# Kernel tuning notes

Measured on AMD Instinct MI355X. Metric: run time of the kernel, lower is better.

The kernel has to match this reference:

```python
import jax, jax.numpy as jnp
import numpy as np

NEG_SLOPE = 0.2  # GATv2Conv default negative_slope
EPS = 1e-5       # BatchNorm1d default eps


def _bn(x, g, b):
    # training-mode batch norm (biased variance, matching torch normalization)
    m = x.mean(0)
    v = x.var(0)
    return (x - m) / jnp.sqrt(v + EPS) * g + b


def setup_inputs() -> dict:
    key = jax.random.key(0)
    N, E, AIN, EIN, HID, H, OUT = 50000, 400000, 64, 16, 64, 8, 1
    ks = jax.random.split(key, 16)
    def nrm(k, shape, s=0.05):
        return jax.random.normal(k, shape, jnp.float32) * s
    return dict(
        x=nrm(ks[0], (N, AIN), 1.0),
        edge_index=jax.random.randint(ks[1], (2, E), 0, N),
        edge_attr=nrm(ks[2], (E, EIN), 1.0),
        W_ap=nrm(ks[3], (AIN, HID)), b_ap=jnp.zeros((HID,), jnp.float32),
        W_ep=nrm(ks[4], (EIN, HID)), b_ep=jnp.zeros((HID,), jnp.float32),
        W_msg=nrm(ks[5], (HID, HID)), b_msg=jnp.zeros((HID,), jnp.float32),
        g_msg=jnp.ones((HID,), jnp.float32), be_msg=jnp.zeros((HID,), jnp.float32),
        W_l=nrm(ks[6], (2 * HID, H * HID)), W_r=nrm(ks[7], (2 * HID, H * HID)),
        att=nrm(ks[8], (H, HID)), b_gat=jnp.zeros((H * HID,), jnp.float32),
        g_bn=jnp.ones((H * HID,), jnp.float32), be_bn=jnp.zeros((H * HID,), jnp.float32),
        W_p1=nrm(ks[9], (H * HID, HID)), b_p1=jnp.zeros((HID,), jnp.float32),
        g_p=jnp.ones((HID,), jnp.float32), be_p=jnp.zeros((HID,), jnp.float32),
        W_p2=nrm(ks[10], (HID, OUT)), b_p2=jnp.zeros((OUT,), jnp.float32),
    )


def reference(x, edge_index, edge_attr,
              W_ap, b_ap, W_ep, b_ep, W_msg, b_msg, g_msg, be_msg,
              W_l, W_r, att, b_gat, g_bn, be_bn,
              W_p1, b_p1, g_p, be_p, W_p2, b_p2):
    N = x.shape[0]
    H, C = att.shape
    row, col = edge_index[0], edge_index[1]

    atom = x @ W_ap + b_ap                      # [N, HID]
    ef = edge_attr @ W_ep + b_ep                # [E, HID]

    # scatter_mean of edge features onto destination nodes
    s = jax.ops.segment_sum(ef, col, num_segments=N)
    cnt = jax.ops.segment_sum(jnp.ones((ef.shape[0],), ef.dtype), col, num_segments=N)
    agg = s / jnp.clip(cnt, 1.0)[:, None]       # [N, HID]

    msg = jax.nn.relu(_bn((atom + agg) @ W_msg + b_msg, g_msg, be_msg))
    comb = jnp.concatenate([msg, agg], axis=1)  # [N, 2*HID]

    # GATv2Conv with default add_self_loops=True, concat=True
    src = jnp.concatenate([row, jnp.arange(N, dtype=row.dtype)])
    dst = jnp.concatenate([col, jnp.arange(N, dtype=col.dtype)])
    xl = (comb @ W_l).reshape(N, H, C)          # source transform
    xr = (comb @ W_r).reshape(N, H, C)          # target transform
    e = jax.nn.leaky_relu(xl[src] + xr[dst], NEG_SLOPE)   # [E+N, H, C]
    score = jnp.einsum('ehc,hc->eh', e, att)               # [E+N, H]
    smax = jax.ops.segment_max(score, dst, num_segments=N)
    ex = jnp.exp(score - smax[dst])
    denom = jax.ops.segment_sum(ex, dst, num_segments=N)
    alpha = ex / denom[dst]                                 # per-dst softmax
    out = jax.ops.segment_sum(alpha[:, :, None] * xl[src], dst, num_segments=N)
    out = out.reshape(N, H * C) + b_gat                     # [N, H*C]

    out = jax.nn.relu(_bn(out, g_bn, be_bn))
    h = jax.nn.relu(_bn(out @ W_p1 + b_p1, g_p, be_p))
    return (h @ W_p2 + b_p2).squeeze(-1)                    # [N]
```

## Files before the change

### kernel.cpp

```cpp
#include <hip/hip_runtime.h>
#include <hip/hip_bf16.h>


#define CDIV(a, b) (((a) + (b) - 1) / (b))

using f32x4 = __attribute__((ext_vector_type(4))) float;
using s16x8 = __attribute__((ext_vector_type(8))) short;
using u32x4 = __attribute__((ext_vector_type(4))) unsigned;

__device__ inline unsigned short f2bf(float f) {
    union { float f; unsigned u; } v; v.f = f;
    unsigned r = v.u + 0x7fff + ((v.u >> 16) & 1);
    return (unsigned short)(r >> 16);
}
__device__ inline float bf_lo(unsigned w) {
    union { unsigned u; float f; } v; v.u = w << 16; return v.f;
}
__device__ inline float bf_hi(unsigned w) {
    union { unsigned u; float f; } v; v.u = w & 0xffff0000u; return v.f;
}
__device__ inline void unp8(u32x4 u, float* v) {
    v[0] = bf_lo(u.x); v[1] = bf_hi(u.x); v[2] = bf_lo(u.y); v[3] = bf_hi(u.y);
    v[4] = bf_lo(u.z); v[5] = bf_hi(u.z); v[6] = bf_lo(u.w); v[7] = bf_hi(u.w);
}

__global__ void k_scatter16(const float* __restrict__ EA, const int* __restrict__ ei,
                            float* __restrict__ agg16, int* __restrict__ cntI, int E) {
    int t = blockIdx.x * blockDim.x + threadIdx.x;
    int e = t >> 4, ch = t & 15;
    if (e >= E) return;
    int dst = ei[E + e];
    float v = __builtin_nontemporal_load(EA + (size_t)e * 16 + ch);
    atomicAdd(&agg16[(size_t)dst * 16 + ch], v);
    if (ch == 0) atomicAdd(&cntI[dst], 1);
}

__global__ void k_prep(const float* __restrict__ Wl, const float* __restrict__ Wr,
                       const float* __restrict__ Wp1, const float* __restrict__ Wap,
                       const float* __restrict__ Wmsg, const float* __restrict__ bap,
                       const float* __restrict__ bmsg, unsigned short* __restrict__ Wt,
                       unsigned short* __restrict__ Wp1t, unsigned short* __restrict__ Wzt,
                       float* __restrict__ bc) {
    int b = blockIdx.x, t = threadIdx.x;
    if (b < 512) {
        int idx = b * 256 + t;
        int c = idx >> 7, k = idx & 127;
        float v = (c < 512) ? Wl[(size_t)k * 512 + c] : Wr[(size_t)k * 512 + (c - 512)];
        Wt[idx] = f2bf(v);
    } else if (b < 640) {
        int idx = (b - 512) * 256 + t;
        int c = idx >> 9, k = idx & 511;
        Wp1t[idx] = f2bf(Wp1[(size_t)k * 64 + c]);
    } else {
        for (int e = t; e < 4096; e += 256) {
            int i = e >> 6, c = e & 63;
            float s = 0.f;
            for (int j = 0; j < 64; ++j) s += Wap[i * 64 + j] * Wmsg[j * 64 + c];
            Wzt[c * 128 + i] = f2bf(s);
        }
        for (int e = t; e < 4096; e += 256) {
            int k = e >> 6, c = e & 63;
            Wzt[c * 128 + 64 + k] = f2bf(Wmsg[k * 64 + c]);
        }
        if (t < 64) {
            float s = bmsg[t];
            for (int j = 0; j < 64; ++j) s += bap[j] * Wmsg[j * 64 + t];
            bc[t] = s;
        }
    }
}

__global__ void k_combin(const float* __restrict__ x, const float* __restrict__ agg16,
                         const int* __restrict__ cntI, const float* __restrict__ Wep,
                         const float* __restrict__ bep, unsigned* __restrict__ combin32,
                         int N) {
    int wid = (blockIdx.x * blockDim.x + threadIdx.x) >> 6;
    int lane = threadIdx.x & 63;
    if (wid >= N) return;
    int c = cntI[wid];
    float mval = (lane < 16 && c > 0) ? agg16[(size_t)wid * 16 + lane] / (float)c : 0.f;
    float aggv = bep[lane];
#pragma unroll
    for (int j = 0; j < 16; ++j) {
        float mj = __shfl(mval, j, 64);
        aggv = fmaf(mj, Wep[j * 64 + lane], aggv);
    }
    if (c == 0) aggv = 0.f;
    float xv = __builtin_nontemporal_load(x + (size_t)wid * 64 + lane);
    int i0 = (lane & 31) * 2;
    float ax = __shfl(xv, i0, 64);
    float bx = __shfl(xv, i0 + 1, 64);
    float aa = __shfl(aggv, i0, 64);
    float ba = __shfl(aggv, i0 + 1, 64);
    float a = (lane < 32) ? ax : aa;
    float b = (lane < 32) ? bx : ba;
    combin32[(size_t)wid * 64 + lane] = (unsigned)f2bf(a) | ((unsigned)f2bf(b) << 16);
}

__global__ __launch_bounds__(256) void k_z(
    const unsigned short* __restrict__ combin, const unsigned short* __restrict__ Wzt,
    const float* __restrict__ bc, float* __restrict__ z, float* __restrict__ sums, int N) {
    __shared__ unsigned short a_lds[64 * 128];
    __shared__ unsigned short b_lds[64 * 128];
    __shared__ float redS[64], redQ[64];
    int t = threadIdx.x;
    int row0 = blockIdx.x * 64;
    for (int i = t; i < 1024; i += 256) {
        int row = i >> 4, seg = i & 15;
        int dsts = (row * 256 + ((seg * 16) ^ ((row & 7) << 4))) >> 1;
        int gr = row0 + row;
        s16x8 v = (s16x8)0;
        if (gr < N) v = *(const s16x8*)(combin + (size_t)gr * 128 + seg * 8);
        *(s16x8*)(a_lds + dsts) = v;
        *(s16x8*)(b_lds + dsts) = *(const s16x8*)(Wzt + (size_t)row * 128 + seg * 8);
    }
    if (t < 64) { redS[t] = 0.f; redQ[t] = 0.f; }
    __syncthreads();
    int w = t >> 6, l = t & 63, hi = l >> 4, lo = l & 15;
    int ar = w * 16 + lo;
    s16x8 a[4];
#pragma unroll
    for (int kk = 0; kk < 4; ++kk) {
        int byte = (kk * 64 + hi * 16) ^ ((ar & 7) << 4);
        a[kk] = *(const s16x8*)(a_lds + ((ar * 256 + byte) >> 1));
    }
#pragma unroll
    for (int cf = 0; cf < 4; ++cf) {
        int br = cf * 16 + lo;
        f32x4 acc = (f32x4){0.f, 0.f, 0.f, 0.f};
#pragma unroll
        for (int kk = 0; kk < 4; ++kk) {
            int byte = (kk * 64 + hi * 16) ^ ((br & 7) << 4);
            s16x8 b = *(const s16x8*)(b_lds + ((br * 256 + byte) >> 1));
            acc = __builtin_amdgcn_mfma_f32_16x16x32_bf16(a[kk], b, acc, 0, 0, 0);
        }
        int colg = cf * 16 + lo;
        float bcv = bc[colg];
        float sv = 0.f, qv = 0.f;
#pragma unroll
        for (int r = 0; r < 4; ++r) {
            int rowg = row0 + w * 16 + hi * 4 + r;
            if (rowg < N) {
                float v = acc[r] + bcv;
                z[(size_t)rowg * 64 + colg] = v;
                sv += v; qv += v * v;
            }
        }
        atomicAdd(&redS[colg], sv);
        atomicAdd(&redQ[colg], qv);
    }
    __syncthreads();
    if (t < 64) {
        atomicAdd(&sums[t], redS[t]);
        atomicAdd(&sums[64 + t], redQ[t]);
    }
}

__global__ __launch_bounds__(256) void k_statsg(const u32x4* __restrict__ X,
                                                float* __restrict__ sums, int N) {
    __shared__ float redS[512], redQ[512];
    int t = threadIdx.x;
    for (int i = t; i < 512; i += 256) { redS[i] = 0.f; redQ[i] = 0.f; }
    __syncthreads();
    int qu = t & 63;
    int slice = (blockIdx.x << 2) | (t >> 6);
    int nsl = gridDim.x << 2;
    float s[8], q[8];
#pragma unroll
    for (int j = 0; j < 8; ++j) { s[j] = 0.f; q[j] = 0.f; }
    for (int n = slice; n < N; n += nsl) {
        u32x4 u = X[(size_t)n * 64 + qu];
        unsigned uu[4] = {u.x, u.y, u.z, u.w};
#pragma unroll
        for (int k2 = 0; k2 < 4; ++k2) {
            float a = bf_lo(uu[k2]), b = bf_hi(uu[k2]);
            s[2 * k2] += a; q[2 * k2] += a * a;
            s[2 * k2 + 1] += b; q[2 * k2 + 1] += b * b;
        }
    }
#pragma unroll
    for (int j = 0; j < 8; ++j) {
        atomicAdd(&redS[qu * 8 + j], s[j]);
        atomicAdd(&redQ[qu * 8 + j], q[j]);
    }
    __syncthreads();
    for (int i = t; i < 512; i += 256) {
        atomicAdd(&sums[i], redS[i]);
        atomicAdd(&sums[512 + i], redQ[i]);
    }
}

__global__ void k_comb2(const float* __restrict__ z, const float* __restrict__ sums,
                        const float* __restrict__ g, const float* __restrict__ be,
                        unsigned* __restrict__ combin32, int N) {
    int idx = blockIdx.x * blockDim.x + threadIdx.x;
    if (idx >= N * 16) return;
    int n = idx >> 4, kq = idx & 15;
    float invN = 1.0f / (float)N;
    float4 zv = *(const float4*)(z + (size_t)n * 64 + kq * 4);
    float zz[4] = {zv.x, zv.y, zv.z, zv.w};
    unsigned h[2];
#pragma unroll
    for (int p = 0; p < 2; ++p) {
        unsigned short w[2];
#pragma unroll
        for (int j = 0; j < 2; ++j) {
            int k = kq * 4 + p * 2 + j;
            float mean = sums[k] * invN;
            float var = sums[64 + k] * invN - mean * mean;
            float s = g[k] * rsqrtf(var + 1e-5f);
            float v = fmaxf(fmaf(zz[p * 2 + j], s, be[k] - mean * s), 0.f);
            w[j] = f2bf(v);
        }
        h[p] = (unsigned)w[0] | ((unsigned)w[1] << 16);
    }
    *(uint2*)(combin32 + (size_t)n * 64 + kq * 2) = make_uint2(h[0], h[1]);
}

__global__ void k_bsum(const int* __restrict__ cntI, int* __restrict__ bsum, int N) {
    int b = blockIdx.x, t = threadIdx.x;
    int base = b * 1024 + t * 4;
    int s = 0;
#pragma unroll
    for (int j = 0; j < 4; ++j) { int i = base + j; if (i < N) s += cntI[i]; }
    for (int off = 32; off; off >>= 1) s += __shfl_xor(s, off, 64);
    __shared__ int wsum[4];
    if ((t & 63) == 0) wsum[t >> 6] = s;
    __syncthreads();
    if (t == 0) bsum[b] = wsum[0] + wsum[1] + wsum[2] + wsum[3];
}
__global__ void k_boff(const int* __restrict__ bsum, int* __restrict__ boff, int nb) {
    int t = threadIdx.x;
    if (t < nb) { int s = 0; for (int j = 0; j < t; ++j) s += bsum[j]; boff[t] = s; }
}
__global__ void k_scan2(const int* __restrict__ cntI, const int* __restrict__ boff,
                        int* __restrict__ rowptr, int N) {
    int b = blockIdx.x, t = threadIdx.x;
    int base = b * 1024 + t * 4;
    int v[4]; int s = 0;
#pragma unroll
    for (int j = 0; j < 4; ++j) { int i = base + j; v[j] = (i < N) ? cntI[i] : 0; s += v[j]; }
    __shared__ int ls[256];
    ls[t] = s; __syncthreads();
    for (int off = 1; off < 256; off <<= 1) {
        int tv = (t >= (int)off) ? ls[t - off] : 0;
        __syncthreads(); ls[t] += tv; __syncthreads();
    }
    int run = ls[t] - s + boff[b];
#pragma unroll
    for (int j = 0; j < 4; ++j) { run += v[j]; int i = base + j; if (i < N) rowptr[i + 1] = run; }
    if (b == 0 && t == 0) rowptr[0] = 0;
}

__global__ void k_fill(const int* __restrict__ ei, const int* __restrict__ rowptr,
                       int* __restrict__ cursor, int* __restrict__ esrc, int E) {
    int e = blockIdx.x * blockDim.x + threadIdx.x;
    if (e >= E) return;
    int dst = ei[E + e];
    int pos = rowptr[dst] + atomicAdd(&cursor[dst], 1);
    esrc[pos] = ei[e];
}

__global__ __launch_bounds__(256) void k_xlxr2(
    const unsigned short* __restrict__ combin, const unsigned short* __restrict__ Wt,
    unsigned short* __restrict__ xlr, int N) {
    __shared__ unsigned short a_lds[64 * 128];
    __shared__ unsigned short b_lds[256 * 128];
    int t = threadIdx.x;
    int row0 = blockIdx.x * 64;
    int c0 = blockIdx.y * 256;
    for (int i = t; i < 1024; i += 256) {
        int row = i >> 4, seg = i & 15;
        int dsts = (row * 256 + ((seg * 16) ^ ((row & 7) << 4))) >> 1;
        int gr = row0 + row;
        s16x8 v = (s16x8)0;
        if (gr < N) v = *(const s16x8*)(combin + (size_t)gr * 128 + seg * 8);
        *(s16x8*)(a_lds + dsts) = v;
    }
    for (int i = t; i < 4096; i += 256) {
        int row = i >> 4, seg = i & 15;
        int dsts = (row * 256 + ((seg * 16) ^ ((row & 7) << 4))) >> 1;
        *(s16x8*)(b_lds + dsts) = *(const s16x8*)(Wt + (size_t)(c0 + row) * 128 + seg * 8);
    }
    __syncthreads();
    int w = t >> 6, l = t & 63, hi = l >> 4, lo = l & 15;
    int ar = w * 16 + lo;
    s16x8 a[4];
#pragma unroll
    for (int kk = 0; kk < 4; ++kk) {
        int byte = (kk * 64 + hi * 16) ^ ((ar & 7) << 4);
        a[kk] = *(const s16x8*)(a_lds + ((ar * 256 + byte) >> 1));
    }
#pragma unroll
    for (int cf = 0; cf < 16; ++cf) {
        int br = cf * 16 + lo;
        f32x4 acc = (f32x4){0.f, 0.f, 0.f, 0.f};
#pragma unroll
        for (int kk = 0; kk < 4; ++kk) {
            int byte = (kk * 64 + hi * 16) ^ ((br & 7) << 4);
            s16x8 b = *(const s16x8*)(b_lds + ((br * 256 + byte) >> 1));
            acc = __builtin_amdgcn_mfma_f32_16x16x32_bf16(a[kk], b, acc, 0, 0, 0);
        }
        int colg = c0 + cf * 16 + lo;
#pragma unroll
        for (int r = 0; r < 4; ++r) {
            int rowg = row0 + w * 16 + hi * 4 + r;
            if (rowg < N) xlr[(size_t)rowg * 1024 + colg] = f2bf(acc[r]);
        }
    }
}

__global__ __launch_bounds__(256) void k_gat(
    const unsigned short* __restrict__ xlr, unsigned* __restrict__ gout32,
    const int* __restrict__ rowptr, const int* __restrict__ esrc,
    const float* __restrict__ att, const float* __restrict__ bg, int N) {
    int wid = (blockIdx.x * blockDim.x + threadIdx.x) >> 6;
    int lane = threadIdx.x & 63;
    if (wid >= N) return;
    int n = wid;
    float xrv[8], av[8], acc[8];
    {
        u32x4 u = __builtin_nontemporal_load(
            (const u32x4*)(xlr + (size_t)n * 1024 + 512 + lane * 8));
        unp8(u, xrv);
    }
#pragma unroll
    for (int j = 0; j < 8; ++j) { av[j] = att[lane * 8 + j]; acc[j] = 0.f; }
    float s = 0.f;
    int e0 = rowptr[n], e1 = rowptr[n + 1];
    int m = e1 - e0 + 1;
    int i = 0;
    for (; i + 2 <= m; i += 2) {
        int ia = e0 + i, ib = e0 + i + 1;
        int s0 = (ia < e1) ? esrc[ia] : n;
        int s1 = (ib < e1) ? esrc[ib] : n;
        u32x4 u0 = *(const u32x4*)(xlr + (size_t)s0 * 1024 + lane * 8);
        u32x4 u1 = *(const u32x4*)(xlr + (size_t)s1 * 1024 + lane * 8);
        float xlv0[8], xlv1[8];
        unp8(u0, xlv0); unp8(u1, xlv1);
        float ps0 = 0.f, ps1 = 0.f;
#pragma unroll
        for (int j = 0; j < 8; ++j) {
            float t0 = xlv0[j] + xrv[j];
            float t1 = xlv1[j] + xrv[j];
            t0 = fmaf(0.4f, fabsf(t0), 0.6f * t0);
            t1 = fmaf(0.4f, fabsf(t1), 0.6f * t1);
            ps0 = fmaf(t0, av[j], ps0);
            ps1 = fmaf(t1, av[j], ps1);
        }
        ps0 += __shfl_xor(ps0, 1, 64); ps1 += __shfl_xor(ps1, 1, 64);
        ps0 += __shfl_xor(ps0, 2, 64); ps1 += __shfl_xor(ps1, 2, 64);
        ps0 += __shfl_xor(ps0, 4, 64); ps1 += __shfl_xor(ps1, 4, 64);
        float w0 = __expf(ps0), w1 = __expf(ps1);
        s += w0 + w1;
#pragma unroll
        for (int j = 0; j < 8; ++j) {
            acc[j] = fmaf(w0, xlv0[j], acc[j]);
            acc[j] = fmaf(w1, xlv1[j], acc[j]);
        }
    }
    if (i < m) {
        int ia = e0 + i;
        int s0 = (ia < e1) ? esrc[ia] : n;
        u32x4 u0 = *(const u32x4*)(xlr + (size_t)s0 * 1024 + lane * 8);
        float xlv0[8];
        unp8(u0, xlv0);
        float ps0 = 0.f;
#pragma unroll
        for (int j = 0; j < 8; ++j) {
            float t0 = xlv0[j] + xrv[j];
            t0 = fmaf(0.4f, fabsf(t0), 0.6f * t0);
            ps0 = fmaf(t0, av[j], ps0);
        }
        ps0 += __shfl_xor(ps0, 1, 64);
        ps0 += __shfl_xor(ps0, 2, 64);
        ps0 += __shfl_xor(ps0, 4, 64);
        float w0 = __expf(ps0);
        s += w0;
#pragma unroll
        for (int j = 0; j < 8; ++j) acc[j] = fmaf(w0, xlv0[j], acc[j]);
    }
    float invs = 1.0f / s;
    u32x4 o;
    {
        float lo0 = acc[0] * invs + bg[lane * 8 + 0];
        float hi0 = acc[1] * invs + bg[lane * 8 + 1];
        float lo1 = acc[2] * invs + bg[lane * 8 + 2];
        float hi1 = acc[3] * invs + bg[lane * 8 + 3];
        float lo2 = acc[4] * invs + bg[lane * 8 + 4];
        float hi2 = acc[5] * invs + bg[lane * 8 + 5];
        float lo3 = acc[6] * invs + bg[lane * 8 + 6];
        float hi3 = acc[7] * invs + bg[lane * 8 + 7];
        o.x = (unsigned)f2bf(lo0) | ((unsigned)f2bf(hi0) << 16);
        o.y = (unsigned)f2bf(lo1) | ((unsigned)f2bf(hi1) << 16);
        o.z = (unsigned)f2bf(lo2) | ((unsigned)f2bf(hi2) << 16);
        o.w = (unsigned)f2bf(lo3) | ((unsigned)f2bf(hi3) << 16);
    }
    __builtin_nontemporal_store(o, (u32x4*)(gout32 + (size_t)n * 256 + lane * 4));
}

__global__ __launch_bounds__(256) void k_postm(
    const unsigned* __restrict__ gout32, const unsigned short* __restrict__ Wp1t,
    const float* __restrict__ gsums, const float* __restrict__ g,
    const float* __restrict__ be, const float* __restrict__ bp1,
    float* __restrict__ h1, float* __restrict__ sums, int N) {
    __shared__ unsigned short a_lds[64 * 128];
    __shared__ unsigned short b_lds[64 * 128];
    __shared__ float sc_l[512], sh_l[512];
    __shared__ float redS[64], redQ[64];
    int t = threadIdx.x;
    float invN = 1.0f / (float)N;
    for (int i = t; i < 512; i += 256) {
        float mean = gsums[i] * invN;
        float var = gsums[512 + i] * invN - mean * mean;
        float s = g[i] * rsqrtf(var + 1e-5f);
        sc_l[i] = s;
        sh_l[i] = be[i] - mean * s;
    }
    if (t < 64) { redS[t] = 0.f; redQ[t] = 0.f; }
    int row0 = blockIdx.x * 64;
    int w = t >> 6, l = t & 63, hi = l >> 4, lo = l & 15;
    int ar = w * 16 + lo;
    f32x4 acc[4];
#pragma unroll
    for (int cf = 0; cf < 4; ++cf) acc[cf] = (f32x4){0.f, 0.f, 0.f, 0.f};
    for (int kc = 0; kc < 4; ++kc) {
        __syncthreads();
        for (int i = t; i < 1024; i += 256) {
            int row = i >> 4, seg = i & 15;
            int dsts = (row * 256 + ((seg * 16) ^ ((row & 7) << 4))) >> 1;
            int gr = row0 + row;
            int k0 = kc * 128 + seg * 8;
            s16x8 v = (s16x8)0;
            if (gr < N) {
                u32x4 u = *(const u32x4*)(gout32 + (size_t)gr * 256 + (k0 >> 1));
                float f[8];
                unp8(u, f);
#pragma unroll
                for (int j = 0; j < 8; ++j) {
                    float y = fmaxf(fmaf(f[j], sc_l[k0 + j], sh_l[k0 + j]), 0.f);
                    v[j] = (short)f2bf(y);
                }
            }
            *(s16x8*)(a_lds + dsts) = v;
            *(s16x8*)(b_lds + dsts) = *(const s16x8*)(Wp1t + (size_t)row * 512 + k0);
        }
        __syncthreads();
        s16x8 a[4];
#pragma unroll
        for (int kk = 0; kk < 4; ++kk) {
            int byte = (kk * 64 + hi * 16) ^ ((ar & 7) << 4);
            a[kk] = *(const s16x8*)(a_lds + ((ar * 256 + byte) >> 1));
        }
#pragma unroll
        for (int cf = 0; cf < 4; ++cf) {
            int br = cf * 16 + lo;
#pragma unroll
            for (int kk = 0; kk < 4; ++kk) {
                int byte = (kk * 64 + hi * 16) ^ ((br & 7) << 4);
                s16x8 b = *(const s16x8*)(b_lds + ((br * 256 + byte) >> 1));
                acc[cf] = __builtin_amdgcn_mfma_f32_16x16x32_bf16(a[kk], b, acc[cf], 0, 0, 0);
            }
        }
    }
#pragma unroll
    for (int cf = 0; cf < 4; ++cf) {
        int colg = cf * 16 + lo;
        float bv = bp1[colg];
        float sv = 0.f, qv = 0.f;
#pragma unroll
        for (int r = 0; r < 4; ++r) {
            int rowg = row0 + w * 16 + hi * 4 + r;
            if (rowg < N) {
                float v = acc[cf][r] + bv;
                h1[(size_t)rowg * 64 + colg] = v;
                sv += v; qv += v * v;
            }
        }
        atomicAdd(&redS[colg], sv);
        atomicAdd(&redQ[colg], qv);
    }
    __syncthreads();
    if (t < 64) {
        atomicAdd(&sums[t], redS[t]);
        atomicAdd(&sums[64 + t], redQ[t]);
    }
}

__global__ void k_final(const float* __restrict__ h1, const float* __restrict__ stats,
                        const float* __restrict__ g, const float* __restrict__ be,
                        const float* __restrict__ Wp2, const float* __restrict__ bp2,
                        float* __restrict__ out, int N) {
    int wid = (blockIdx.x * blockDim.x + threadIdx.x) >> 6;
    int lane = threadIdx.x & 63;
    if (wid >= N) return;
    float invN = 1.0f / (float)N;
    float mean = stats[lane] * invN;
    float var = stats[64 + lane] * invN - mean * mean;
    float inv = rsqrtf(var + 1e-5f);
    float v = h1[(size_t)wid * 64 + lane];
    v = fmaxf((v - mean) * (inv * g[lane]) + be[lane], 0.f);
    float p = v * Wp2[lane];
#pragma unroll
    for (int off = 32; off; off >>= 1) p += __shfl_xor(p, off, 64);
    if (lane == 0) out[wid] = p + bp2[0];
}

extern "C" void kernel_launch(void* const* d_in, const int* in_sizes, int n_in,
                              void* d_out, int out_size, void* d_ws, size_t ws_size,
                              hipStream_t stream) {
    const float* x      = (const float*)d_in[0];
    const int*   ei     = (const int*)d_in[1];
    const float* ea     = (const float*)d_in[2];
    const float* W_ap   = (const float*)d_in[3];
    const float* b_ap   = (const float*)d_in[4];
    const float* W_ep   = (const float*)d_in[5];
    const float* b_ep   = (const float*)d_in[6];
    const float* W_msg  = (const float*)d_in[7];
    const float* b_msg  = (const float*)d_in[8];
    const float* g_msg  = (const float*)d_in[9];
    const float* be_msg = (const float*)d_in[10];
    const float* W_l    = (const float*)d_in[11];
    const float* W_r    = (const float*)d_in[12];
    const float* att    = (const float*)d_in[13];
    const float* b_gat  = (const float*)d_in[14];
    const float* g_bn   = (const float*)d_in[15];
    const float* be_bn  = (const float*)d_in[16];
    const float* W_p1   = (const float*)d_in[17];
    const float* b_p1   = (const float*)d_in[18];
    const float* g_p    = (const float*)d_in[19];
    const float* be_p   = (const float*)d_in[20];
    const float* W_p2   = (const float*)d_in[21];
    const float* b_p2   = (const float*)d_in[22];

    int N = in_sizes[0] / 64;
    int E = in_sizes[1] / 2;
    int nb = CDIV(N, 1024);

    float* ws = (float*)d_ws;
    size_t off = 0;
    float* agg16  = ws + off; off += (size_t)N * 16;
    int*   cntI   = (int*)(ws + off); off += N;
    int*   cursor = (int*)(ws + off); off += N;
    float* st_msg = ws + off; off += 128;
    float* st_gat = ws + off; off += 1024;
    float* st_p   = ws + off; off += 128;
    size_t zero_floats = off;
    unsigned short* combin = (unsigned short*)(ws + off); off += (size_t)N * 64;
    float* zb     = ws + off; off += (size_t)N * 64;
    unsigned short* Wzt = (unsigned short*)(ws + off); off += 4096;
    float* bc     = ws + off; off += 64;
    int*   rowptr = (int*)(ws + off); off += (size_t)(N + 1); off = (off + 3) & ~(size_t)3;
    int*   esrc   = (int*)(ws + off); off += E;
    int*   bsum   = (int*)(ws + off); off += 64;
    int*   boff   = (int*)(ws + off); off += 64;
    unsigned short* Wt  = (unsigned short*)(ws + off); off += 65536;
    unsigned short* Wp1t = (unsigned short*)(ws + off); off += 16384;
    unsigned short* xlr = (unsigned short*)(ws + off); off += (size_t)N * 512;
    unsigned* gout32 = (unsigned*)(ws + off); off += (size_t)N * 256;
    float* h1 = zb;

    hipMemsetAsync(d_ws, 0, zero_floats * sizeof(float), stream);

    k_prep<<<641, 256, 0, stream>>>(W_l, W_r, W_p1, W_ap, W_msg, b_ap, b_msg,
                                    Wt, Wp1t, Wzt, bc);
    k_scatter16<<<CDIV(E * 16, 256), 256, 0, stream>>>(ea, ei, agg16, cntI, E);
    k_combin<<<CDIV(N * 64, 256), 256, 0, stream>>>(x, agg16, cntI, W_ep, b_ep,
                                                    (unsigned*)combin, N);
    k_z<<<CDIV(N, 64), 256, 0, stream>>>(combin, Wzt, bc, zb, st_msg, N);
    k_comb2<<<CDIV(N * 16, 256), 256, 0, stream>>>(zb, st_msg, g_msg, be_msg,
                                                   (unsigned*)combin, N);
    k_bsum<<<nb, 256, 0, stream>>>(cntI, bsum, N);
    k_boff<<<1, 64, 0, stream>>>(bsum, boff, nb);
    k_scan2<<<nb, 256, 0, stream>>>(cntI, boff, rowptr, N);
    k_fill<<<CDIV(E, 256), 256, 0, stream>>>(ei, rowptr, cursor, esrc, E);
    dim3 gx(CDIV(N, 64), 4);
    k_xlxr2<<<gx, 256, 0, stream>>>(combin, Wt, xlr, N);
    k_gat<<<CDIV(N * 64, 256), 256, 0, stream>>>(xlr, gout32, rowptr, esrc, att, b_gat, N);
    k_statsg<<<256, 256, 0, stream>>>((const u32x4*)gout32, st_gat, N);
    k_postm<<<CDIV(N, 64), 256, 0, stream>>>(gout32, Wp1t, st_gat, g_bn, be_bn,
                                             b_p1, h1, st_p, N);
    k_final<<<CDIV(N * 64, 256), 256, 0, stream>>>(h1, st_p, g_p, be_p, W_p2, b_p2,
                                                   (float*)d_out, N);
}
```

Before: 408.0 us.

## Replace atomic edge-feature scatter with CSR gather and batch GAT index loads

The per-channel atomicAdd scatter of edge features is removed. The CSR build (count, scan, fill) now runs first and also records original edge ids, so k_combin gathers and averages edge attributes per destination node without atomics. The GAT kernel loads 64 source indices per wave at once, broadcasts them with shuffles, and unrolls four edges to raise memory-level parallelism. It also uses a simpler leaky-relu, vectorized att/bias loads, and drops the nontemporal hints. This adds an extra E-sized index array and a random gather of edge_attr rows.

```diff
diff --git a/kernel.cpp b/kernel.cpp
--- a/kernel.cpp
+++ b/kernel.cpp
@@ -24,15 +24,10 @@
     v[4] = bf_lo(u.z); v[5] = bf_hi(u.z); v[6] = bf_lo(u.w); v[7] = bf_hi(u.w);
 }
 
-__global__ void k_scatter16(const float* __restrict__ EA, const int* __restrict__ ei,
-                            float* __restrict__ agg16, int* __restrict__ cntI, int E) {
-    int t = blockIdx.x * blockDim.x + threadIdx.x;
-    int e = t >> 4, ch = t & 15;
+__global__ void k_count(const int* __restrict__ ei, int* __restrict__ cntI, int E) {
+    int e = blockIdx.x * blockDim.x + threadIdx.x;
     if (e >= E) return;
-    int dst = ei[E + e];
-    float v = __builtin_nontemporal_load(EA + (size_t)e * 16 + ch);
-    atomicAdd(&agg16[(size_t)dst * 16 + ch], v);
-    if (ch == 0) atomicAdd(&cntI[dst], 1);
+    atomicAdd(&cntI[ei[E + e]], 1);
 }
 
 __global__ void k_prep(const float* __restrict__ Wl, const float* __restrict__ Wr,
@@ -70,23 +65,76 @@
     }
 }
 
-__global__ void k_combin(const float* __restrict__ x, const float* __restrict__ agg16,
-                         const int* __restrict__ cntI, const float* __restrict__ Wep,
-                         const float* __restrict__ bep, unsigned* __restrict__ combin32,
-                         int N) {
+__global__ void k_bsum(const int* __restrict__ cntI, int* __restrict__ bsum, int N) {
+    int b = blockIdx.x, t = threadIdx.x;
+    int base = b * 1024 + t * 4;
+    int s = 0;
+#pragma unroll
+    for (int j = 0; j < 4; ++j) { int i = base + j; if (i < N) s += cntI[i]; }
+    for (int off = 32; off; off >>= 1) s += __shfl_xor(s, off, 64);
+    __shared__ int wsum[4];
+    if ((t & 63) == 0) wsum[t >> 6] = s;
+    __syncthreads();
+    if (t == 0) bsum[b] = wsum[0] + wsum[1] + wsum[2] + wsum[3];
+}
+__global__ void k_boff(const int* __restrict__ bsum, int* __restrict__ boff, int nb) {
+    int t = threadIdx.x;
+    if (t < nb) { int s = 0; for (int j = 0; j < t; ++j) s += bsum[j]; boff[t] = s; }
+}
+__global__ void k_scan2(const int* __restrict__ cntI, const int* __restrict__ boff,
+                        int* __restrict__ rowptr, int N) {
+    int b = blockIdx.x, t = threadIdx.x;
+    int base = b * 1024 + t * 4;
+    int v[4]; int s = 0;
+#pragma unroll
+    for (int j = 0; j < 4; ++j) { int i = base + j; v[j] = (i < N) ? cntI[i] : 0; s += v[j]; }
+    __shared__ int ls[256];
+    ls[t] = s; __syncthreads();
+    for (int off = 1; off < 256; off <<= 1) {
+        int tv = (t >= (int)off) ? ls[t - off] : 0;
+        __syncthreads(); ls[t] += tv; __syncthreads();
+    }
+    int run = ls[t] - s + boff[b];
+#pragma unroll
+    for (int j = 0; j < 4; ++j) { run += v[j]; int i = base + j; if (i < N) rowptr[i + 1] = run; }
+    if (b == 0 && t == 0) rowptr[0] = 0;
+}
+
+__global__ void k_fill(const int* __restrict__ ei, const int* __restrict__ rowptr,
+                       int* __restrict__ cursor, int* __restrict__ esrc,
+                       int* __restrict__ eidx, int E) {
+    int e = blockIdx.x * blockDim.x + threadIdx.x;
+    if (e >= E) return;
+    int dst = ei[E + e];
+    int pos = rowptr[dst] + atomicAdd(&cursor[dst], 1);
+    esrc[pos] = ei[e];
+    eidx[pos] = e;
+}
+
+__global__ void k_combin(const float* __restrict__ x, const float* __restrict__ ea,
+                         const int* __restrict__ rowptr, const int* __restrict__ eidx,
+                         const float* __restrict__ Wep, const float* __restrict__ bep,
+                         unsigned* __restrict__ combin32, int N) {
     int wid = (blockIdx.x * blockDim.x + threadIdx.x) >> 6;
     int lane = threadIdx.x & 63;
     if (wid >= N) return;
-    int c = cntI[wid];
-    float mval = (lane < 16 && c > 0) ? agg16[(size_t)wid * 16 + lane] / (float)c : 0.f;
+    int e0 = rowptr[wid], e1 = rowptr[wid + 1];
+    int deg = e1 - e0;
+    int le = lane >> 4, ch = lane & 15;
+    float part = 0.f;
+    for (int p = e0 + le; p < e1; p += 4)
+        part += ea[(size_t)eidx[p] * 16 + ch];
+    part += __shfl_xor(part, 16, 64);
+    part += __shfl_xor(part, 32, 64);
+    float mval = (deg > 0) ? part / (float)deg : 0.f;
     float aggv = bep[lane];
 #pragma unroll
     for (int j = 0; j < 16; ++j) {
         float mj = __shfl(mval, j, 64);
         aggv = fmaf(mj, Wep[j * 64 + lane], aggv);
     }
-    if (c == 0) aggv = 0.f;
-    float xv = __builtin_nontemporal_load(x + (size_t)wid * 64 + lane);
+    if (deg == 0) aggv = 0.f;
+    float xv = x[(size_t)wid * 64 + lane];
     int i0 = (lane & 31) * 2;
     float ax = __shfl(xv, i0, 64);
     float bx = __shfl(xv, i0 + 1, 64);
@@ -217,50 +265,6 @@
     *(uint2*)(combin32 + (size_t)n * 64 + kq * 2) = make_uint2(h[0], h[1]);
 }
 
-__global__ void k_bsum(const int* __restrict__ cntI, int* __restrict__ bsum, int N) {
-    int b = blockIdx.x, t = threadIdx.x;
-    int base = b * 1024 + t * 4;
-    int s = 0;
-#pragma unroll
-    for (int j = 0; j < 4; ++j) { int i = base + j; if (i < N) s += cntI[i]; }
-    for (int off = 32; off; off >>= 1) s += __shfl_xor(s, off, 64);
-    __shared__ int wsum[4];
-    if ((t & 63) == 0) wsum[t >> 6] = s;
-    __syncthreads();
-    if (t == 0) bsum[b] = wsum[0] + wsum[1] + wsum[2] + wsum[3];
-}
-__global__ void k_boff(const int* __restrict__ bsum, int* __restrict__ boff, int nb) {
-    int t = threadIdx.x;
-    if (t < nb) { int s = 0; for (int j = 0; j < t; ++j) s += bsum[j]; boff[t] = s; }
-}
-__global__ void k_scan2(const int* __restrict__ cntI, const int* __restrict__ boff,
-                        int* __restrict__ rowptr, int N) {
-    int b = blockIdx.x, t = threadIdx.x;
-    int base = b * 1024 + t * 4;
-    int v[4]; int s = 0;
-#pragma unroll
-    for (int j = 0; j < 4; ++j) { int i = base + j; v[j] = (i < N) ? cntI[i] : 0; s += v[j]; }
-    __shared__ int ls[256];
-    ls[t] = s; __syncthreads();
-    for (int off = 1; off < 256; off <<= 1) {
-        int tv = (t >= (int)off) ? ls[t - off] : 0;
-        __syncthreads(); ls[t] += tv; __syncthreads();
-    }
-    int run = ls[t] - s + boff[b];
-#pragma unroll
-    for (int j = 0; j < 4; ++j) { run += v[j]; int i = base + j; if (i < N) rowptr[i + 1] = run; }
-    if (b == 0 && t == 0) rowptr[0] = 0;
-}
-
-__global__ void k_fill(const int* __restrict__ ei, const int* __restrict__ rowptr,
-                       int* __restrict__ cursor, int* __restrict__ esrc, int E) {
-    int e = blockIdx.x * blockDim.x + threadIdx.x;
-    if (e >= E) return;
-    int dst = ei[E + e];
-    int pos = rowptr[dst] + atomicAdd(&cursor[dst], 1);
-    esrc[pos] = ei[e];
-}
-
 __global__ __launch_bounds__(256) void k_xlxr2(
     const unsigned short* __restrict__ combin, const unsigned short* __restrict__ Wt,
     unsigned short* __restrict__ xlr, int N) {
@@ -310,6 +314,26 @@
     }
 }
 
+__device__ inline void gat_edge(u32x4 u, const float* xrv, const float* av,
+                                float* acc, float& s) {
+    float xlv[8];
+    unp8(u, xlv);
+    float ps = 0.f;
+#pragma unroll
+    for (int j = 0; j < 8; ++j) {
+        float t = xlv[j] + xrv[j];
+        t = fmaxf(t, 0.2f * t);
+        ps = fmaf(t, av[j], ps);
+    }
+    ps += __shfl_xor(ps, 1, 64);
+    ps += __shfl_xor(ps, 2, 64);
+    ps += __shfl_xor(ps, 4, 64);
+    float w = __expf(ps);
+    s += w;
+#pragma unroll
+    for (int j = 0; j < 8; ++j) acc[j] = fmaf(w, xlv[j], acc[j]);
+}
+
 __global__ __launch_bounds__(256) void k_gat(
     const unsigned short* __restrict__ xlr, unsigned* __restrict__ gout32,
     const int* __restrict__ rowptr, const int* __restrict__ esrc,
@@ -320,83 +344,67 @@
     int n = wid;
     float xrv[8], av[8], acc[8];
     {
-        u32x4 u = __builtin_nontemporal_load(
-            (const u32x4*)(xlr + (size_t)n * 1024 + 512 + lane * 8));
+        u32x4 u = *(const u32x4*)(xlr + (size_t)n * 1024 + 512 + lane * 8);
         unp8(u, xrv);
     }
-#pragma unroll
-    for (int j = 0; j < 8; ++j) { av[j] = att[lane * 8 + j]; acc[j] = 0.f; }
+    {
+        float4 a0 = *(const float4*)(att + lane * 8);
+        float4 a1 = *(const float4*)(att + lane * 8 + 4);
+        av[0] = a0.x; av[1] = a0.y; av[2] = a0.z; av[3] = a0.w;
+        av[4] = a1.x; av[5] = a1.y; av[6] = a1.z; av[7] = a1.w;
+    }
+#pragma unroll
+    for (int j = 0; j < 8; ++j) acc[j] = 0.f;
     float s = 0.f;
     int e0 = rowptr[n], e1 = rowptr[n + 1];
     int m = e1 - e0 + 1;
-    int i = 0;
-    for (; i + 2 <= m; i += 2) {
-        int ia = e0 + i, ib = e0 + i + 1;
-        int s0 = (ia < e1) ? esrc[ia] : n;
-        int s1 = (ib < e1) ? esrc[ib] : n;
-        u32x4 u0 = *(const u32x4*)(xlr + (size_t)s0 * 1024 + lane * 8);
-        u32x4 u1 = *(const u32x4*)(xlr + (size_t)s1 * 1024 + lane * 8);
-        float xlv0[8], xlv1[8];
-        unp8(u0, xlv0); unp8(u1, xlv1);
-        float ps0 = 0.f, ps1 = 0.f;
-#pragma unroll
-        for (int j = 0; j < 8; ++j) {
-            float t0 = xlv0[j] + xrv[j];
-            float t1 = xlv1[j] + xrv[j];
-            t0 = fmaf(0.4f, fabsf(t0), 0.6f * t0);
-            t1 = fmaf(0.4f, fabsf(t1), 0.6f * t1);
-            ps0 = fmaf(t0, av[j], ps0);
-            ps1 = fmaf(t1, av[j], ps1);
-        }
-        ps0 += __shfl_xor(ps0, 1, 64); ps1 += __shfl_xor(ps1, 1, 64);
-        ps0 += __shfl_xor(ps0, 2, 64); ps1 += __shfl_xor(ps1, 2, 64);
-        ps0 += __shfl_xor(ps0, 4, 64); ps1 += __shfl_xor(ps1, 4, 64);
-        float w0 = __expf(ps0), w1 = __expf(ps1);
-        s += w0 + w1;
-#pragma unroll
-        for (int j = 0; j < 8; ++j) {
-            acc[j] = fmaf(w0, xlv0[j], acc[j]);
-            acc[j] = fmaf(w1, xlv1[j], acc[j]);
-        }
-    }
-    if (i < m) {
-        int ia = e0 + i;
-        int s0 = (ia < e1) ? esrc[ia] : n;
-        u32x4 u0 = *(const u32x4*)(xlr + (size_t)s0 * 1024 + lane * 8);
-        float xlv0[8];
-        unp8(u0, xlv0);
-        float ps0 = 0.f;
-#pragma unroll
-        for (int j = 0; j < 8; ++j) {
-            float t0 = xlv0[j] + xrv[j];
-            t0 = fmaf(0.4f, fabsf(t0), 0.6f * t0);
-            ps0 = fmaf(t0, av[j], ps0);
-        }
-        ps0 += __shfl_xor(ps0, 1, 64);
-        ps0 += __shfl_xor(ps0, 2, 64);
-        ps0 += __shfl_xor(ps0, 4, 64);
-        float w0 = __expf(ps0);
-        s += w0;
-#pragma unroll
-        for (int j = 0; j < 8; ++j) acc[j] = fmaf(w0, xlv0[j], acc[j]);
+    for (int base = 0; base < m; base += 64) {
+        int ie = e0 + base + lane;
+        int myIdx = (ie < e1) ? esrc[ie] : n;
+        int cnt = min(64, m - base);
+        int i = 0;
+        for (; i + 4 <= cnt; i += 4) {
+            int s0 = __shfl(myIdx, i, 64);
+            int s1 = __shfl(myIdx, i + 1, 64);
+            int s2 = __shfl(myIdx, i + 2, 64);
+            int s3 = __shfl(myIdx, i + 3, 64);
+            u32x4 u0 = *(const u32x4*)(xlr + (size_t)s0 * 1024 + lane * 8);
+            u32x4 u1 = *(const u32x4*)(xlr + (size_t)s1 * 1024 + lane * 8);
+            u32x4 u2 = *(const u32x4*)(xlr + (size_t)s2 * 1024 + lane * 8);
+            u32x4 u3 = *(const u32x4*)(xlr + (size_t)s3 * 1024 + lane * 8);
+            gat_edge(u0, xrv, av, acc, s);
+            gat_edge(u1, xrv, av, acc, s);
+            gat_edge(u2, xrv, av, acc, s);
+            gat_edge(u3, xrv, av, acc, s);
+        }
+        for (; i + 2 <= cnt; i += 2) {
+            int s0 = __shfl(myIdx, i, 64);
+            int s1 = __shfl(myIdx, i + 1, 64);
+            u32x4 u0 = *(const u32x4*)(xlr + (size_t)s0 * 1024 + lane * 8);
+            u32x4 u1 = *(const u32x4*)(xlr + (size_t)s1 * 1024 + lane * 8);
+            gat_edge(u0, xrv, av, acc, s);
+            gat_edge(u1, xrv, av, acc, s);
+        }
+        if (i < cnt) {
+            int s0 = __shfl(myIdx, i, 64);
+            u32x4 u0 = *(const u32x4*)(xlr + (size_t)s0 * 1024 + lane * 8);
+            gat_edge(u0, xrv, av, acc, s);
+        }
     }
     float invs = 1.0f / s;
+    float bgv[8];
+    {
+        float4 b0 = *(const float4*)(bg + lane * 8);
+        float4 b1 = *(const float4*)(bg + lane * 8 + 4);
+        bgv[0] = b0.x; bgv[1] = b0.y; bgv[2] = b0.z; bgv[3] = b0.w;
+        bgv[4] = b1.x; bgv[5] = b1.y; bgv[6] = b1.z; bgv[7] = b1.w;
+    }
     u32x4 o;
-    {
-        float lo0 = acc[0] * invs + bg[lane * 8 + 0];
-        float hi0 = acc[1] * invs + bg[lane * 8 + 1];
-        float lo1 = acc[2] * invs + bg[lane * 8 + 2];
-        float hi1 = acc[3] * invs + bg[lane * 8 + 3];
-        float lo2 = acc[4] * invs + bg[lane * 8 + 4];
-        float hi2 = acc[5] * invs + bg[lane * 8 + 5];
-        float lo3 = acc[6] * invs + bg[lane * 8 + 6];
-        float hi3 = acc[7] * invs + bg[lane * 8 + 7];
-        o.x = (unsigned)f2bf(lo0) | ((unsigned)f2bf(hi0) << 16);
-        o.y = (unsigned)f2bf(lo1) | ((unsigned)f2bf(hi1) << 16);
-        o.z = (unsigned)f2bf(lo2) | ((unsigned)f2bf(hi2) << 16);
-        o.w = (unsigned)f2bf(lo3) | ((unsigned)f2bf(hi3) << 16);
-    }
-    __builtin_nontemporal_store(o, (u32x4*)(gout32 + (size_t)n * 256 + lane * 4));
+    o.x = (unsigned)f2bf(acc[0] * invs + bgv[0]) | ((unsigned)f2bf(acc[1] * invs + bgv[1]) << 16);
+    o.y = (unsigned)f2bf(acc[2] * invs + bgv[2]) | ((unsigned)f2bf(acc[3] * invs + bgv[3]) << 16);
+    o.z = (unsigned)f2bf(acc[4] * invs + bgv[4]) | ((unsigned)f2bf(acc[5] * invs + bgv[5]) << 16);
+    o.w = (unsigned)f2bf(acc[6] * invs + bgv[6]) | ((unsigned)f2bf(acc[7] * invs + bgv[7]) << 16);
+    *(u32x4*)(gout32 + (size_t)n * 256 + lane * 4) = o;
 }
 
 __global__ __launch_bounds__(256) void k_postm(
@@ -539,7 +547,6 @@
 
     float* ws = (float*)d_ws;
     size_t off = 0;
-    float* agg16  = ws + off; off += (size_t)N * 16;
     int*   cntI   = (int*)(ws + off); off += N;
     int*   cursor = (int*)(ws + off); off += N;
     float* st_msg = ws + off; off += 128;
@@ -552,6 +559,7 @@
     float* bc     = ws + off; off += 64;
     int*   rowptr = (int*)(ws + off); off += (size_t)(N + 1); off = (off + 3) & ~(size_t)3;
     int*   esrc   = (int*)(ws + off); off += E;
+    int*   eidx   = (int*)(ws + off); off += E;
     int*   bsum   = (int*)(ws + off); off += 64;
     int*   boff   = (int*)(ws + off); off += 64;
     unsigned short* Wt  = (unsigned short*)(ws + off); off += 65536;
@@ -564,16 +572,16 @@
 
     k_prep<<<641, 256, 0, stream>>>(W_l, W_r, W_p1, W_ap, W_msg, b_ap, b_msg,
                                     Wt, Wp1t, Wzt, bc);
-    k_scatter16<<<CDIV(E * 16, 256), 256, 0, stream>>>(ea, ei, agg16, cntI, E);
-    k_combin<<<CDIV(N * 64, 256), 256, 0, stream>>>(x, agg16, cntI, W_ep, b_ep,
+    k_count<<<CDIV(E, 256), 256, 0, stream>>>(ei, cntI, E);
+    k_bsum<<<nb, 256, 0, stream>>>(cntI, bsum, N);
+    k_boff<<<1, 64, 0, stream>>>(bsum, boff, nb);
+    k_scan2<<<nb, 256, 0, stream>>>(cntI, boff, rowptr, N);
+    k_fill<<<CDIV(E, 256), 256, 0, stream>>>(ei, rowptr, cursor, esrc, eidx, E);
+    k_combin<<<CDIV(N * 64, 256), 256, 0, stream>>>(x, ea, rowptr, eidx, W_ep, b_ep,
                                                     (unsigned*)combin, N);
     k_z<<<CDIV(N, 64), 256, 0, stream>>>(combin, Wzt, bc, zb, st_msg, N);
     k_comb2<<<CDIV(N * 16, 256), 256, 0, stream>>>(zb, st_msg, g_msg, be_msg,
                                                    (unsigned*)combin, N);
-    k_bsum<<<nb, 256, 0, stream>>>(cntI, bsum, N);
-    k_boff<<<1, 64, 0, stream>>>(bsum, boff, nb);
-    k_scan2<<<nb, 256, 0, stream>>>(cntI, boff, rowptr, N);
-    k_fill<<<CDIV(E, 256), 256, 0, stream>>>(ei, rowptr, cursor, esrc, E);
     dim3 gx(CDIV(N, 64), 4);
     k_xlxr2<<<gx, 256, 0, stream>>>(combin, Wt, xlr, N);
     k_gat<<<CDIV(N * 64, 256), 256, 0, stream>>>(xlr, gout32, rowptr, esrc, att, b_gat, N);
```

Result: faster. 384.2 us (-5.8%).
